# Kernel tuning notes

Hardware: AMD Instinct MI355X
Metric: run time of the kernel (lower is better)

The kernel has to match this reference:

```python
import jax, jax.numpy as jnp
import numpy as np

B, S, HID = 2, 2048, 1024
H, D = 16, 64  # num query heads, head_dim; single shared KV head
SCALE = D ** -0.5


def setup_inputs() -> dict:
    key = jax.random.key(0)
    k1, k2, k3, k4, k5 = jax.random.split(key, 5)
    return {
        "hidden_states": jax.random.normal(k1, (B, S, HID), dtype=jnp.float32),
        "Wq": jax.random.normal(k2, (HID, HID), dtype=jnp.float32) * 0.02,
        "Wk": jax.random.normal(k3, (HID, D), dtype=jnp.float32) * 0.02,
        "Wv": jax.random.normal(k4, (HID, D), dtype=jnp.float32) * 0.02,
        "Wo": jax.random.normal(k5, (HID, HID), dtype=jnp.float32) * 0.02,
    }


def reference(hidden_states, Wq, Wk, Wv, Wo):
    b, s, _ = hidden_states.shape
    # projections: Q has H heads; K/V have a single shared head of dim D
    q = (hidden_states @ Wq).reshape(b, s, H, D)  # [B,S,H,D]
    k = hidden_states @ Wk                        # [B,S,D]
    v = hidden_states @ Wv                        # [B,S,D]
    # scores: broadcast single KV head across all query heads
    scores = jnp.einsum("bqhd,bkd->bhqk", q, k) * SCALE  # [B,H,S,S]
    attn = jax.nn.softmax(scores, axis=-1)
    out = jnp.einsum("bhqk,bkd->bqhd", attn, v).reshape(b, s, HID)
    return out @ Wo
```

## Files before the change

kernel.cpp:

```cpp
#include <hip/hip_runtime.h>
#include <math.h>

#define BATCH 2
#define SEQ   2048
#define HID   1024
#define NH    16
#define HD    64
#define MTOT  (BATCH * SEQ)

#define PST 72
#define VST 88
#define WTS 69

#define EXP_C1 0.1803368801111255f
#define EXP_C2 (-17.312340490667562f)

typedef __attribute__((ext_vector_type(8))) short short8;
typedef __attribute__((ext_vector_type(4))) short short4v;
typedef __attribute__((ext_vector_type(4))) float floatx4;

#if __has_builtin(__builtin_amdgcn_mfma_f32_16x16x16bf16_1k)
#define MFMA16(a, b, c) __builtin_amdgcn_mfma_f32_16x16x16bf16_1k(a, b, c, 0, 0, 0)
#else
static __device__ __forceinline__ floatx4 mfma16_asm(short4v a, short4v b, floatx4 c) {
    floatx4 d;
    asm("v_mfma_f32_16x16x16_bf16 %0, %1, %2, %3" : "=&v"(d) : "v"(a), "v"(b), "v"(c));
    return d;
}
#define MFMA16(a, b, c) mfma16_asm(a, b, c)
#endif

__device__ __forceinline__ unsigned short f2bf(float x) {
    unsigned u = __float_as_uint(x);
    u += 0x7FFF + ((u >> 16) & 1);
    return (unsigned short)(u >> 16);
}
__device__ __forceinline__ float bf2f(unsigned short h) {
    return __uint_as_float((unsigned)h << 16);
}
__device__ __forceinline__ void split16(const float* f, unsigned short* hh, unsigned short* ll) {
    #pragma unroll
    for (int e = 0; e < 16; ++e) {
        unsigned short h = f2bf(f[e]);
        hh[e] = h;
        ll[e] = f2bf(f[e] - bf2f(h));
    }
}

__global__ __launch_bounds__(256)
void presplit_kernel(const float* __restrict__ Wq, const float* __restrict__ Wk,
                     const float* __restrict__ Wv, const float* __restrict__ Wo,
                     const float* __restrict__ X,
                     unsigned short* __restrict__ WqTh, unsigned short* __restrict__ WqTl,
                     unsigned short* __restrict__ WkTh, unsigned short* __restrict__ WkTl,
                     unsigned short* __restrict__ WvTh, unsigned short* __restrict__ WvTl,
                     unsigned short* __restrict__ WoTh, unsigned short* __restrict__ WoTl,
                     unsigned short* __restrict__ Xh)
{
    __shared__ __align__(16) float Wtmp[64][WTS];
    const int tid = threadIdx.x;
    int bx = blockIdx.x;

    if (bx >= 544) {
        size_t i0 = (size_t)(bx - 544) * 4096 + tid * 16;
        float f[16];
        *(float4*)&f[0]  = *(const float4*)(X + i0 + 0);
        *(float4*)&f[4]  = *(const float4*)(X + i0 + 4);
        *(float4*)&f[8]  = *(const float4*)(X + i0 + 8);
        *(float4*)&f[12] = *(const float4*)(X + i0 + 12);
        unsigned short hh[16];
        #pragma unroll
        for (int e = 0; e < 16; ++e) hh[e] = f2bf(f[e]);
        *(uint4*)(Xh + i0)     = *(uint4*)&hh[0];
        *(uint4*)(Xh + i0 + 8) = *(uint4*)&hh[8];
        return;
    }

    const float* W; unsigned short *Th, *Tl; int ldw, kt, nt;
    if (bx < 256)      { W = Wq; Th = WqTh; Tl = WqTl; ldw = HID; kt = bx >> 4; nt = bx & 15; }
    else if (bx < 272) { W = Wk; Th = WkTh; Tl = WkTl; ldw = HD;  kt = bx - 256; nt = 0; }
    else if (bx < 288) { W = Wv; Th = WvTh; Tl = WvTl; ldw = HD;  kt = bx - 272; nt = 0; }
    else               { W = Wo; Th = WoTh; Tl = WoTl; ldw = HID; bx -= 288; kt = bx >> 4; nt = bx & 15; }
    const int k0 = kt * 64, n0 = nt * 64;

    {
        const int wk = tid >> 2, wn = (tid & 3) * 16;
        const float* wp = W + (size_t)(k0 + wk) * ldw + n0 + wn;
        float f[16];
        *(float4*)&f[0]  = *(const float4*)(wp + 0);
        *(float4*)&f[4]  = *(const float4*)(wp + 4);
        *(float4*)&f[8]  = *(const float4*)(wp + 8);
        *(float4*)&f[12] = *(const float4*)(wp + 12);
        #pragma unroll
        for (int e = 0; e < 16; ++e) Wtmp[wk][wn + e] = f[e];
    }
    __syncthreads();
    {
        const int rn = tid >> 2, rk = (tid & 3) * 16;
        float f[16];
        #pragma unroll
        for (int e = 0; e < 16; ++e) f[e] = Wtmp[rk + e][rn];
        unsigned short hh[16], ll[16];
        split16(f, hh, ll);
        size_t off = (size_t)(n0 + rn) * HID + k0 + rk;
        *(uint4*)(Th + off)     = *(uint4*)&hh[0];
        *(uint4*)(Th + off + 8) = *(uint4*)&hh[8];
        *(uint4*)(Tl + off)     = *(uint4*)&ll[0];
        *(uint4*)(Tl + off + 8) = *(uint4*)&ll[8];
    }
}

__global__ __launch_bounds__(256)
void qkv_kernel(const unsigned short* __restrict__ Xh,
                const unsigned short* __restrict__ WqTh, const unsigned short* __restrict__ WqTl,
                const unsigned short* __restrict__ WkTh, const unsigned short* __restrict__ WkTl,
                const unsigned short* __restrict__ WvTh, const unsigned short* __restrict__ WvTl,
                unsigned short* __restrict__ Qh,
                unsigned short* __restrict__ Kh, unsigned short* __restrict__ Vth)
{
    __shared__ __align__(16) unsigned short Ah[128][PST];
    __shared__ __align__(16) unsigned short Wsh[64][PST], Wsl[64][PST];

    const int tid  = threadIdx.x;
    const int wave = tid >> 6, lane = tid & 63;
    const int t = lane & 15, quad = lane >> 4;
    const int m0 = blockIdx.x * 128;
    const int nb = blockIdx.y;

    const unsigned short *WTh, *WTl; int n0b;
    if (nb < 16)       { WTh = WqTh; WTl = WqTl; n0b = nb * 64; }
    else if (nb == 16) { WTh = WkTh; WTl = WkTl; n0b = 0; }
    else               { WTh = WvTh; WTl = WvTl; n0b = 0; }

    floatx4 acc[2][4];
    #pragma unroll
    for (int mi = 0; mi < 2; ++mi)
        #pragma unroll
        for (int sub = 0; sub < 4; ++sub) acc[mi][sub] = (floatx4){0.f,0.f,0.f,0.f};

    for (int kt = 0; kt < HID / 64; ++kt) {
        __syncthreads();
        #pragma unroll
        for (int i = 0; i < 4; ++i) {
            int c = tid + i * 256;
            int row = c >> 3, col8 = (c & 7) * 8;
            *(uint4*)&Ah[row][col8] =
                *(const uint4*)(Xh + (size_t)(m0 + row) * HID + kt * 64 + col8);
        }
        #pragma unroll
        for (int i = 0; i < 2; ++i) {
            int c = tid + i * 256;
            int row = c >> 3, col8 = (c & 7) * 8;
            size_t g = (size_t)(n0b + row) * HID + kt * 64 + col8;
            *(uint4*)&Wsh[row][col8] = *(const uint4*)(WTh + g);
            *(uint4*)&Wsl[row][col8] = *(const uint4*)(WTl + g);
        }
        __syncthreads();
        #pragma unroll
        for (int ks = 0; ks < 2; ++ks) {
            short8 bh[4], bl[4];
            #pragma unroll
            for (int sub = 0; sub < 4; ++sub) {
                bh[sub] = *(const short8*)&Wsh[sub * 16 + t][ks * 32 + quad * 8];
                bl[sub] = *(const short8*)&Wsl[sub * 16 + t][ks * 32 + quad * 8];
            }
            #pragma unroll
            for (int mi = 0; mi < 2; ++mi) {
                short8 ah = *(const short8*)&Ah[wave * 32 + mi * 16 + t][ks * 32 + quad * 8];
                #pragma unroll
                for (int sub = 0; sub < 4; ++sub) {
                    acc[mi][sub] = __builtin_amdgcn_mfma_f32_16x16x32_bf16(ah, bh[sub], acc[mi][sub], 0, 0, 0);
                    acc[mi][sub] = __builtin_amdgcn_mfma_f32_16x16x32_bf16(ah, bl[sub], acc[mi][sub], 0, 0, 0);
                }
            }
        }
    }

    #pragma unroll
    for (int mi = 0; mi < 2; ++mi)
        #pragma unroll
        for (int sub = 0; sub < 4; ++sub)
            #pragma unroll
            for (int r = 0; r < 4; ++r) {
                int g = m0 + wave * 32 + mi * 16 + quad * 4 + r;
                int d = sub * 16 + t;
                unsigned short hh = f2bf(acc[mi][sub][r]);
                if (nb < 16) {
                    int b = g >> 11, s = g & (SEQ - 1);
                    Qh[((size_t)(b * NH + nb) * SEQ + s) * HD + d] = hh;
                } else if (nb == 16) {
                    Kh[(size_t)g * HD + d] = hh;
                } else {
                    int b = g >> 11, s = g & (SEQ - 1);
                    Vth[(size_t)b * HD * SEQ + (size_t)d * SEQ + s] = hh;
                }
            }
}

__global__ __launch_bounds__(512, 4)
void flash_kernel(const unsigned short* __restrict__ Qhg,
                  const unsigned short* __restrict__ Khg,
                  const unsigned short* __restrict__ Vthg,
                  unsigned short* __restrict__ Oh)
{
    __shared__ __align__(16) unsigned short Ksh[64][PST];
    __shared__ __align__(16) unsigned short Vsh[64][VST];

    const int tid  = threadIdx.x;
    const int wave = tid >> 6, lane = tid & 63;
    const int t = lane & 15, quad = lane >> 4;

    const int q0 = blockIdx.x * 128;
    const int h  = blockIdx.y;
    const int b  = blockIdx.z;

    short8 qf[2];
    {
        const unsigned short* qp =
            Qhg + ((size_t)(b * NH + h) * SEQ + q0 + wave * 16 + t) * HD + quad * 8;
        qf[0] = *(const short8*)(qp);
        qf[1] = *(const short8*)(qp + 32);
    }

    const unsigned short* Kh_b  = Khg  + (size_t)b * SEQ * HD;
    const unsigned short* Vth_b = Vthg + (size_t)b * HD * SEQ;

    const int srow = tid >> 3, scol = (tid & 7) * 8;

    float l_part = 0.f;
    floatx4 o[4];
    #pragma unroll
    for (int dsub = 0; dsub < 4; ++dsub) o[dsub] = (floatx4){0.f,0.f,0.f,0.f};

    for (int kt = 0; kt < SEQ / 64; ++kt) {
        __syncthreads();
        *(uint4*)&Ksh[srow][scol] =
            *(const uint4*)(Kh_b + (size_t)(kt * 64 + srow) * HD + scol);
        *(uint4*)&Vsh[srow][scol] =
            *(const uint4*)(Vth_b + (size_t)srow * SEQ + kt * 64 + scol);
        __syncthreads();

        floatx4 sf[4];
        #pragma unroll
        for (int ksub = 0; ksub < 4; ++ksub) sf[ksub] = (floatx4){0.f,0.f,0.f,0.f};
        #pragma unroll
        for (int dks = 0; dks < 2; ++dks) {
            short8 kf[4];
            #pragma unroll
            for (int ksub = 0; ksub < 4; ++ksub)
                kf[ksub] = *(const short8*)&Ksh[ksub * 16 + t][dks * 32 + quad * 8];
            #pragma unroll
            for (int ksub = 0; ksub < 4; ++ksub)
                sf[ksub] = __builtin_amdgcn_mfma_f32_16x16x32_bf16(kf[ksub], qf[dks], sf[ksub], 0, 0, 0);
        }

        short4v pk[4];
        #pragma unroll
        for (int ksub = 0; ksub < 4; ++ksub)
            #pragma unroll
            for (int r = 0; r < 4; ++r) {
                float e = exp2f(fmaf(sf[ksub][r], EXP_C1, EXP_C2));
                unsigned u = __float_as_uint(e);
                l_part += __uint_as_float(u & 0xFFFF0000u);
                pk[ksub][r] = (short)(u >> 16);
            }

        #pragma unroll
        for (int ksub = 0; ksub < 4; ++ksub) {
            short4v vv[4];
            #pragma unroll
            for (int dsub = 0; dsub < 4; ++dsub)
                vv[dsub] = *(const short4v*)&Vsh[dsub * 16 + t][ksub * 16 + quad * 4];
            #pragma unroll
            for (int dsub = 0; dsub < 4; ++dsub)
                o[dsub] = MFMA16(pk[ksub], vv[dsub], o[dsub]);
        }
    }

    l_part += __shfl_xor(l_part, 16);
    l_part += __shfl_xor(l_part, 32);
    #pragma unroll
    for (int reg = 0; reg < 4; ++reg) {
        float lr  = __shfl(l_part, quad * 4 + reg);
        float inv = 1.0f / lr;
        size_t row = (size_t)(b * SEQ + q0 + wave * 16 + quad * 4 + reg) * HID + h * HD;
        #pragma unroll
        for (int dsub = 0; dsub < 4; ++dsub)
            Oh[row + dsub * 16 + t] = f2bf(o[dsub][reg] * inv);
    }
}

__global__ __launch_bounds__(256)
void out_proj_kernel(const unsigned short* __restrict__ Ohg,
                     const unsigned short* __restrict__ WoTh,
                     const unsigned short* __restrict__ WoTl,
                     float* __restrict__ out)
{
    __shared__ __align__(16) unsigned short Ah[128][PST];
    __shared__ __align__(16) unsigned short Wsh[64][PST], Wsl[64][PST];

    const int tid  = threadIdx.x;
    const int wave = tid >> 6, lane = tid & 63;
    const int t = lane & 15, quad = lane >> 4;
    const int m0 = blockIdx.x * 128;
    const int n0 = blockIdx.y * 64;

    floatx4 acc[2][4];
    #pragma unroll
    for (int mi = 0; mi < 2; ++mi)
        #pragma unroll
        for (int sub = 0; sub < 4; ++sub) acc[mi][sub] = (floatx4){0.f,0.f,0.f,0.f};

    for (int kt = 0; kt < HID / 64; ++kt) {
        __syncthreads();
        #pragma unroll
        for (int i = 0; i < 4; ++i) {
            int c = tid + i * 256;
            int row = c >> 3, col8 = (c & 7) * 8;
            *(uint4*)&Ah[row][col8] =
                *(const uint4*)(Ohg + (size_t)(m0 + row) * HID + kt * 64 + col8);
        }
        #pragma unroll
        for (int i = 0; i < 2; ++i) {
            int c = tid + i * 256;
            int row = c >> 3, col8 = (c & 7) * 8;
            size_t g = (size_t)(n0 + row) * HID + kt * 64 + col8;
            *(uint4*)&Wsh[row][col8] = *(const uint4*)(WoTh + g);
            *(uint4*)&Wsl[row][col8] = *(const uint4*)(WoTl + g);
        }
        __syncthreads();
        #pragma unroll
        for (int ks = 0; ks < 2; ++ks) {
            short8 bh[4], bl[4];
            #pragma unroll
            for (int sub = 0; sub < 4; ++sub) {
                bh[sub] = *(const short8*)&Wsh[sub * 16 + t][ks * 32 + quad * 8];
                bl[sub] = *(const short8*)&Wsl[sub * 16 + t][ks * 32 + quad * 8];
            }
            #pragma unroll
            for (int mi = 0; mi < 2; ++mi) {
                short8 ah = *(const short8*)&Ah[wave * 32 + mi * 16 + t][ks * 32 + quad * 8];
                #pragma unroll
                for (int sub = 0; sub < 4; ++sub) {
                    acc[mi][sub] = __builtin_amdgcn_mfma_f32_16x16x32_bf16(ah, bh[sub], acc[mi][sub], 0, 0, 0);
                    acc[mi][sub] = __builtin_amdgcn_mfma_f32_16x16x32_bf16(ah, bl[sub], acc[mi][sub], 0, 0, 0);
                }
            }
        }
    }

    #pragma unroll
    for (int mi = 0; mi < 2; ++mi)
        #pragma unroll
        for (int sub = 0; sub < 4; ++sub)
            #pragma unroll
            for (int r = 0; r < 4; ++r)
                out[(size_t)(m0 + wave * 32 + mi * 16 + quad * 4 + r) * HID
                    + n0 + sub * 16 + t] = acc[mi][sub][r];
}

extern "C" void kernel_launch(void* const* d_in, const int* in_sizes, int n_in,
                              void* d_out, int out_size, void* d_ws, size_t ws_size,
                              hipStream_t stream)
{
    const float* X  = (const float*)d_in[0];
    const float* Wq = (const float*)d_in[1];
    const float* Wk = (const float*)d_in[2];
    const float* Wv = (const float*)d_in[3];
    const float* Wo = (const float*)d_in[4];
    float* out = (float*)d_out;

    unsigned short* Qh = (unsigned short*)d_out;
    unsigned short* Xh = Qh + (size_t)BATCH * NH * SEQ * HD;

    char* ws = (char*)d_ws;
    const size_t SZ_WQ = (size_t)HID * HID * 2;
    const size_t SZ_WK = (size_t)HD * HID * 2;
    unsigned short* WqTh = (unsigned short*)(ws);
    unsigned short* WqTl = (unsigned short*)(ws + SZ_WQ);
    unsigned short* WkTh = (unsigned short*)(ws + 2*SZ_WQ);
    unsigned short* WkTl = (unsigned short*)(ws + 2*SZ_WQ + SZ_WK);
    unsigned short* WvTh = (unsigned short*)(ws + 2*SZ_WQ + 2*SZ_WK);
    unsigned short* WvTl = (unsigned short*)(ws + 2*SZ_WQ + 3*SZ_WK);
    unsigned short* WoTh = (unsigned short*)(ws + 2*SZ_WQ + 4*SZ_WK);
    unsigned short* WoTl = (unsigned short*)(ws + 3*SZ_WQ + 4*SZ_WK);
    unsigned short* Kh   = (unsigned short*)(ws + 4*SZ_WQ + 4*SZ_WK);
    unsigned short* Vth  = (unsigned short*)(ws + 4*SZ_WQ + 4*SZ_WK + (size_t)MTOT*HD*2);
    unsigned short* Oh   = (unsigned short*)(ws + 4*SZ_WQ + 4*SZ_WK + (size_t)MTOT*HD*4);

    presplit_kernel<<<dim3(1568), 256, 0, stream>>>(Wq, Wk, Wv, Wo, X,
        WqTh, WqTl, WkTh, WkTl, WvTh, WvTl, WoTh, WoTl, Xh);
    qkv_kernel<<<dim3(MTOT / 128, 18), 256, 0, stream>>>(Xh,
        WqTh, WqTl, WkTh, WkTl, WvTh, WvTl, Qh, Kh, Vth);
    flash_kernel<<<dim3(SEQ / 128, NH, BATCH), 512, 0, stream>>>(Qh, Kh, Vth, Oh);
    out_proj_kernel<<<dim3(MTOT / 128, HID / 64), 256, 0, stream>>>(Oh, WoTh, WoTl, out);
}
```

Before: 206.7 us.

## Rewrite flash attention with 32x32 MFMA tiles and register-prefetched K/V

```diff
diff --git a/kernel.cpp b/kernel.cpp
--- a/kernel.cpp
+++ b/kernel.cpp
@@ -9,26 +9,24 @@
 #define MTOT  (BATCH * SEQ)
 
 #define PST 72
-#define VST 88
 #define WTS 69
 
 #define EXP_C1 0.1803368801111255f
 #define EXP_C2 (-17.312340490667562f)
 
 typedef __attribute__((ext_vector_type(8))) short short8;
-typedef __attribute__((ext_vector_type(4))) short short4v;
 typedef __attribute__((ext_vector_type(4))) float floatx4;
-
-#if __has_builtin(__builtin_amdgcn_mfma_f32_16x16x16bf16_1k)
-#define MFMA16(a, b, c) __builtin_amdgcn_mfma_f32_16x16x16bf16_1k(a, b, c, 0, 0, 0)
-#else
-static __device__ __forceinline__ floatx4 mfma16_asm(short4v a, short4v b, floatx4 c) {
-    floatx4 d;
-    asm("v_mfma_f32_16x16x16_bf16 %0, %1, %2, %3" : "=&v"(d) : "v"(a), "v"(b), "v"(c));
-    return d;
-}
-#define MFMA16(a, b, c) mfma16_asm(a, b, c)
-#endif
+typedef __attribute__((ext_vector_type(16))) float floatx16;
+typedef __attribute__((ext_vector_type(4))) unsigned int uint4v;
+
+#define MFMA32(a, b, c) __builtin_amdgcn_mfma_f32_32x32x16_bf16(a, b, c, 0, 0, 0)
+
+static __device__ __forceinline__ floatx16 zero16() {
+    floatx16 z;
+    #pragma unroll
+    for (int i = 0; i < 16; ++i) z[i] = 0.f;
+    return z;
+}
 
 __device__ __forceinline__ unsigned short f2bf(float x) {
     unsigned u = __float_as_uint(x);
@@ -37,6 +35,9 @@
 }
 __device__ __forceinline__ float bf2f(unsigned short h) {
     return __uint_as_float((unsigned)h << 16);
+}
+__device__ __forceinline__ unsigned pack2bf(float lo, float hi) {
+    return (unsigned)f2bf(lo) | ((unsigned)f2bf(hi) << 16);
 }
 __device__ __forceinline__ void split16(const float* f, unsigned short* hh, unsigned short* ll) {
     #pragma unroll
@@ -197,96 +198,114 @@
             }
 }
 
-__global__ __launch_bounds__(512, 4)
+__global__ __launch_bounds__(256, 2)
 void flash_kernel(const unsigned short* __restrict__ Qhg,
                   const unsigned short* __restrict__ Khg,
                   const unsigned short* __restrict__ Vthg,
                   unsigned short* __restrict__ Oh)
 {
     __shared__ __align__(16) unsigned short Ksh[64][PST];
-    __shared__ __align__(16) unsigned short Vsh[64][VST];
+    __shared__ __align__(16) unsigned short Vsh[64][PST];
 
     const int tid  = threadIdx.x;
     const int wave = tid >> 6, lane = tid & 63;
-    const int t = lane & 15, quad = lane >> 4;
+    const int lq = lane & 31, hi = lane >> 5;
 
     const int q0 = blockIdx.x * 128;
     const int h  = blockIdx.y;
     const int b  = blockIdx.z;
 
-    short8 qf[2];
+    short8 qreg[4];
     {
         const unsigned short* qp =
-            Qhg + ((size_t)(b * NH + h) * SEQ + q0 + wave * 16 + t) * HD + quad * 8;
-        qf[0] = *(const short8*)(qp);
-        qf[1] = *(const short8*)(qp + 32);
+            Qhg + ((size_t)(b * NH + h) * SEQ + q0 + wave * 32 + lq) * HD + hi * 8;
+        #pragma unroll
+        for (int dc = 0; dc < 4; ++dc) qreg[dc] = *(const short8*)(qp + dc * 16);
     }
 
     const unsigned short* Kh_b  = Khg  + (size_t)b * SEQ * HD;
     const unsigned short* Vth_b = Vthg + (size_t)b * HD * SEQ;
 
-    const int srow = tid >> 3, scol = (tid & 7) * 8;
+    const int sr = tid >> 3, sc = (tid & 7) * 8;
 
     float l_part = 0.f;
-    floatx4 o[4];
-    #pragma unroll
-    for (int dsub = 0; dsub < 4; ++dsub) o[dsub] = (floatx4){0.f,0.f,0.f,0.f};
+    floatx16 o0 = zero16(), o1 = zero16();
+
+    uint4 gk0 = *(const uint4*)(Kh_b + (size_t)sr * HD + sc);
+    uint4 gk1 = *(const uint4*)(Kh_b + (size_t)(sr + 32) * HD + sc);
+    uint4 gv0 = *(const uint4*)(Vth_b + (size_t)sr * SEQ + sc);
+    uint4 gv1 = *(const uint4*)(Vth_b + (size_t)(sr + 32) * SEQ + sc);
 
     for (int kt = 0; kt < SEQ / 64; ++kt) {
         __syncthreads();
-        *(uint4*)&Ksh[srow][scol] =
-            *(const uint4*)(Kh_b + (size_t)(kt * 64 + srow) * HD + scol);
-        *(uint4*)&Vsh[srow][scol] =
-            *(const uint4*)(Vth_b + (size_t)srow * SEQ + kt * 64 + scol);
-        __syncthreads();
-
-        floatx4 sf[4];
-        #pragma unroll
-        for (int ksub = 0; ksub < 4; ++ksub) sf[ksub] = (floatx4){0.f,0.f,0.f,0.f};
-        #pragma unroll
-        for (int dks = 0; dks < 2; ++dks) {
-            short8 kf[4];
-            #pragma unroll
-            for (int ksub = 0; ksub < 4; ++ksub)
-                kf[ksub] = *(const short8*)&Ksh[ksub * 16 + t][dks * 32 + quad * 8];
-            #pragma unroll
-            for (int ksub = 0; ksub < 4; ++ksub)
-                sf[ksub] = __builtin_amdgcn_mfma_f32_16x16x32_bf16(kf[ksub], qf[dks], sf[ksub], 0, 0, 0);
-        }
-
-        short4v pk[4];
-        #pragma unroll
-        for (int ksub = 0; ksub < 4; ++ksub)
-            #pragma unroll
-            for (int r = 0; r < 4; ++r) {
-                float e = exp2f(fmaf(sf[ksub][r], EXP_C1, EXP_C2));
-                unsigned u = __float_as_uint(e);
-                l_part += __uint_as_float(u & 0xFFFF0000u);
-                pk[ksub][r] = (short)(u >> 16);
-            }
-
-        #pragma unroll
-        for (int ksub = 0; ksub < 4; ++ksub) {
-            short4v vv[4];
-            #pragma unroll
-            for (int dsub = 0; dsub < 4; ++dsub)
-                vv[dsub] = *(const short4v*)&Vsh[dsub * 16 + t][ksub * 16 + quad * 4];
-            #pragma unroll
-            for (int dsub = 0; dsub < 4; ++dsub)
-                o[dsub] = MFMA16(pk[ksub], vv[dsub], o[dsub]);
-        }
-    }
-
-    l_part += __shfl_xor(l_part, 16);
-    l_part += __shfl_xor(l_part, 32);
-    #pragma unroll
-    for (int reg = 0; reg < 4; ++reg) {
-        float lr  = __shfl(l_part, quad * 4 + reg);
-        float inv = 1.0f / lr;
-        size_t row = (size_t)(b * SEQ + q0 + wave * 16 + quad * 4 + reg) * HID + h * HD;
-        #pragma unroll
-        for (int dsub = 0; dsub < 4; ++dsub)
-            Oh[row + dsub * 16 + t] = f2bf(o[dsub][reg] * inv);
+        *(uint4*)&Ksh[sr][sc]      = gk0;
+        *(uint4*)&Ksh[sr + 32][sc] = gk1;
+        *(uint4*)&Vsh[sr][sc]      = gv0;
+        *(uint4*)&Vsh[sr + 32][sc] = gv1;
+        if (kt + 1 < SEQ / 64) {
+            gk0 = *(const uint4*)(Kh_b + (size_t)((kt + 1) * 64 + sr) * HD + sc);
+            gk1 = *(const uint4*)(Kh_b + (size_t)((kt + 1) * 64 + sr + 32) * HD + sc);
+            gv0 = *(const uint4*)(Vth_b + (size_t)sr * SEQ + (kt + 1) * 64 + sc);
+            gv1 = *(const uint4*)(Vth_b + (size_t)(sr + 32) * SEQ + (kt + 1) * 64 + sc);
+        }
+        __syncthreads();
+
+        floatx16 sf0 = zero16(), sf1 = zero16();
+        __builtin_amdgcn_s_setprio(1);
+        #pragma unroll
+        for (int dc = 0; dc < 4; ++dc) {
+            short8 k0 = *(const short8*)&Ksh[lq][dc * 16 + hi * 8];
+            short8 k1 = *(const short8*)&Ksh[32 + lq][dc * 16 + hi * 8];
+            sf0 = MFMA32(k0, qreg[dc], sf0);
+            sf1 = MFMA32(k1, qreg[dc], sf1);
+        }
+        __builtin_amdgcn_s_setprio(0);
+
+        unsigned w0[8], w1[8];
+        #pragma unroll
+        for (int kc = 0; kc < 2; ++kc)
+            #pragma unroll
+            for (int rr = 0; rr < 4; ++rr) {
+                float e0 = exp2f(fmaf(kc ? sf1[rr * 4 + 0] : sf0[rr * 4 + 0], EXP_C1, EXP_C2));
+                float e1 = exp2f(fmaf(kc ? sf1[rr * 4 + 1] : sf0[rr * 4 + 1], EXP_C1, EXP_C2));
+                float e2 = exp2f(fmaf(kc ? sf1[rr * 4 + 2] : sf0[rr * 4 + 2], EXP_C1, EXP_C2));
+                float e3 = exp2f(fmaf(kc ? sf1[rr * 4 + 3] : sf0[rr * 4 + 3], EXP_C1, EXP_C2));
+                l_part += (e0 + e1) + (e2 + e3);
+                w0[kc * 4 + rr] = pack2bf(e0, e1);
+                w1[kc * 4 + rr] = pack2bf(e2, e3);
+            }
+
+        #pragma unroll
+        for (int m = 0; m < 4; ++m) {
+            unsigned send0 = hi ? w0[2 * m] : w0[2 * m + 1];
+            unsigned send1 = hi ? w1[2 * m] : w1[2 * m + 1];
+            unsigned recv0 = (unsigned)__shfl_xor((int)send0, 32);
+            unsigned recv1 = (unsigned)__shfl_xor((int)send1, 32);
+            unsigned own0 = hi ? w0[2 * m + 1] : w0[2 * m];
+            unsigned own1 = hi ? w1[2 * m + 1] : w1[2 * m];
+            uint4v pw;
+            pw.x = hi ? recv0 : own0;
+            pw.y = hi ? recv1 : own1;
+            pw.z = hi ? own0 : recv0;
+            pw.w = hi ? own1 : recv1;
+            short8 pa = __builtin_bit_cast(short8, pw);
+            short8 v0 = *(const short8*)&Vsh[lq][m * 16 + hi * 8];
+            short8 v1 = *(const short8*)&Vsh[32 + lq][m * 16 + hi * 8];
+            __builtin_amdgcn_s_setprio(1);
+            o0 = MFMA32(pa, v0, o0);
+            o1 = MFMA32(pa, v1, o1);
+            __builtin_amdgcn_s_setprio(0);
+        }
+    }
+
+    float l_full = l_part + __shfl_xor(l_part, 32);
+    #pragma unroll
+    for (int r = 0; r < 16; ++r) {
+        int qr = (r & 3) + 8 * (r >> 2) + 4 * hi;
+        float inv = 1.0f / __shfl(l_full, qr);
+        size_t row = (size_t)(b * SEQ + q0 + wave * 32 + qr) * HID + h * HD;
+        Oh[row + lq]      = f2bf(o0[r] * inv);
+        Oh[row + 32 + lq] = f2bf(o1[r] * inv);
     }
 }
 
@@ -392,6 +411,6 @@
         WqTh, WqTl, WkTh, WkTl, WvTh, WvTl, WoTh, WoTl, Xh);
     qkv_kernel<<<dim3(MTOT / 128, 18), 256, 0, stream>>>(Xh,
         WqTh, WqTl, WkTh, WkTl, WvTh, WvTl, Qh, Kh, Vth);
-    flash_kernel<<<dim3(SEQ / 128, NH, BATCH), 512, 0, stream>>>(Qh, Kh, Vth, Oh);
+    flash_kernel<<<dim3(SEQ / 128, NH, BATCH), 256, 0, stream>>>(Qh, Kh, Vth, Oh);
     out_proj_kernel<<<dim3(MTOT / 128, HID / 64), 256, 0, stream>>>(Oh, WoTh, WoTl, out);
 }
```

Measured after the change: 206.1 us. Within noise of the previous version (-0.3%).
